# Kernel tuning notes

Hardware: AMD Instinct MI355X
Metric: run time of the kernel (lower is better)

The kernel has to match this reference:

```python
import jax, jax.numpy as jnp
import numpy as np

B, T = 1024, 128
T_IN, A_IN, V_IN = 300, 74, 35
D = 128            # dim_capsule
H = D // 2
ROUTING = 3
LABEL = 1


def _glorot(key, shape):
    fan_out, fan_in = shape[-2], shape[-1]
    s = jnp.sqrt(2.0 / (fan_in + fan_out)).astype(jnp.float32)
    return jax.random.normal(key, shape, jnp.float32) * s


def setup_inputs() -> dict:
    k = iter(jax.random.split(jax.random.key(0), 40))
    inp = {}
    inp["text"] = jax.random.normal(next(k), (B, T, T_IN), jnp.float32)
    inp["audio"] = jax.random.normal(next(k), (B, T, A_IN), jnp.float32)
    inp["video"] = jax.random.normal(next(k), (B, T, V_IN), jnp.float32)
    # bidirectional encoder LSTMs (hidden = D//2 per direction); biases b = b_ih + b_hh
    for p, din in (("t", T_IN), ("a", A_IN), ("v", V_IN)):
        for d in ("f", "b"):
            inp[p + "_Wih_" + d] = _glorot(next(k), (4 * H, din))
            inp[p + "_Whh_" + d] = _glorot(next(k), (4 * H, H))
            inp[p + "_b_" + d] = jnp.zeros((4 * H,), jnp.float32)
    # 4 capsule projection matrices per modality, stacked [4, D, D]
    inp["Wt"] = _glorot(next(k), (4, D, D))
    inp["Wa"] = _glorot(next(k), (4, D, D))
    inp["Wv"] = _glorot(next(k), (4, D, D))
    # routing LSTMs (ta, tv, av, tav) stacked on leading axis
    inp["r_Wih"] = _glorot(next(k), (4, 4 * D, D))
    inp["r_Whh"] = _glorot(next(k), (4, 4 * D, D))
    inp["r_b"] = jnp.zeros((4, 4 * D), jnp.float32)
    # decision bidirectional LSTM (hidden = D per direction)
    for d in ("f", "b"):
        inp["d_Wih_" + d] = _glorot(next(k), (4 * D, D))
        inp["d_Whh_" + d] = _glorot(next(k), (4 * D, D))
        inp["d_b_" + d] = jnp.zeros((4 * D,), jnp.float32)
    inp["fc1_W"] = _glorot(next(k), (H, D))
    inp["fc1_b"] = jnp.zeros((H,), jnp.float32)
    inp["fc2_W"] = _glorot(next(k), (LABEL, H))
    inp["fc2_b"] = jnp.zeros((LABEL,), jnp.float32)
    inp["batch_size"] = B
    return inp


def _lstm_final(x, Wih, Whh, b):
    # x: [B, T, I] -> final hidden state [B, Hh]; torch gate order i, f, g, o
    Hh = Whh.shape[-1]
    z = jnp.zeros((x.shape[0], Hh), x.dtype)

    def step(carry, xt):
        h, c = carry
        g = xt @ Wih.T + h @ Whh.T + b
        i, f, gg, o = jnp.split(g, 4, axis=-1)
        c = jax.nn.sigmoid(f) * c + jax.nn.sigmoid(i) * jnp.tanh(gg)
        h = jax.nn.sigmoid(o) * jnp.tanh(c)
        return (h, c), None

    (h, _), _ = jax.lax.scan(step, (z, z), jnp.swapaxes(x, 0, 1))
    return h


def _forward(text, audio, video,
             t_Wih_f, t_Whh_f, t_b_f, t_Wih_b, t_Whh_b, t_b_b,
             a_Wih_f, a_Whh_f, a_b_f, a_Wih_b, a_Whh_b, a_b_b,
             v_Wih_f, v_Whh_f, v_b_f, v_Wih_b, v_Whh_b, v_b_b,
             Wt, Wa, Wv, r_Wih, r_Whh, r_b,
             d_Wih_f, d_Whh_f, d_b_f, d_Wih_b, d_Whh_b, d_b_b,
             fc1_W, fc1_b, fc2_W, fc2_b):
    Bsz = text.shape[0]

    def ctx(x, Wf, Uf, bf, Wb, Ub, bb):
        # biLSTM final hidden, fwd||bwd concat -> [B, 1, D]
        hf = _lstm_final(x, Wf, Uf, bf)
        hb = _lstm_final(x[:, ::-1], Wb, Ub, bb)
        return jnp.concatenate([hf, hb], -1)[:, None, :]

    tc = ctx(text, t_Wih_f, t_Whh_f, t_b_f, t_Wih_b, t_Whh_b, t_b_b)
    ac = ctx(audio, a_Wih_f, a_Whh_f, a_b_f, a_Wih_b, a_Whh_b, a_b_b)
    vc = ctx(video, v_Wih_f, v_Whh_f, v_b_f, v_Wih_b, v_Whh_b, v_b_b)

    tusc = jnp.einsum('bod,kde->kboe', tc, Wt)   # [4, B, 1, D]
    ausc = jnp.einsum('bod,kde->kboe', ac, Wa)
    vusc = jnp.einsum('bod,kde->kboe', vc, Wv)

    pre = [jnp.concatenate([tusc[0], ausc[0]], 1),                # ta  [B,2,D]
           jnp.concatenate([tusc[1], vusc[0]], 1),                # tv  [B,2,D]
           jnp.concatenate([ausc[1], vusc[1]], 1),                # av  [B,2,D]
           jnp.concatenate([tusc[2], ausc[2], vusc[2]], 1)]       # tav [B,3,D]

    rc = [jnp.ones((Bsz, n, D), text.dtype) for n in (2, 2, 2, 3, 7)]
    dc = None
    for r in range(ROUTING + 1):
        rc = [jax.nn.softmax(c, axis=1) for c in rc]
        # per-pair routing LSTMs, final hidden [B,1,D]
        bc = [_lstm_final(rc[i] * pre[i], r_Wih[i], r_Whh[i], r_b[i])[:, None, :]
              for i in range(4)]
        deci = jnp.concatenate([tusc[3], ausc[3], vusc[3]] + bc, 1)  # [B,7,D]
        xd = rc[4] * deci
        # decision biLSTM: sum of both directions' final hidden -> [B,1,D]
        dc = (_lstm_final(xd, d_Wih_f, d_Whh_f, d_b_f)
              + _lstm_final(xd[:, ::-1], d_Wih_b, d_Whh_b, d_b_b))[:, None, :]
        if r < ROUTING:
            # agreement update: bmm gives [B,n,1], broadcasts over last dim (== repeat)
            rc = [rc[i] + jnp.matmul(pre[i], jnp.swapaxes(bc[i], 1, 2)) for i in range(4)] \
                 + [rc[4] + jnp.matmul(deci, jnp.swapaxes(dc, 1, 2))]

    dc = dc[:, 0, :]
    o1 = jnp.tanh(dc @ fc1_W.T + fc1_b)
    return o1 @ fc2_W.T + fc2_b   # mosi: no output tanh


def reference(text, audio, video,
              t_Wih_f, t_Whh_f, t_b_f, t_Wih_b, t_Whh_b, t_b_b,
              a_Wih_f, a_Whh_f, a_b_f, a_Wih_b, a_Whh_b, a_b_b,
              v_Wih_f, v_Whh_f, v_b_f, v_Wih_b, v_Whh_b, v_b_b,
              Wt, Wa, Wv, r_Wih, r_Whh, r_b,
              d_Wih_f, d_Whh_f, d_b_f, d_Wih_b, d_Whh_b, d_b_b,
              fc1_W, fc1_b, fc2_W, fc2_b, batch_size):
    return _forward(text, audio, video,
                    t_Wih_f, t_Whh_f, t_b_f, t_Wih_b, t_Whh_b, t_b_b,
                    a_Wih_f, a_Whh_f, a_b_f, a_Wih_b, a_Whh_b, a_b_b,
                    v_Wih_f, v_Whh_f, v_b_f, v_Wih_b, v_Whh_b, v_b_b,
                    Wt, Wa, Wv, r_Wih, r_Whh, r_b,
                    d_Wih_f, d_Whh_f, d_b_f, d_Wih_b, d_Whh_b, d_b_b,
                    fc1_W, fc1_b, fc2_W, fc2_b)
```

## Files before the change

### kernel.cpp

```cpp
#include <hip/hip_runtime.h>

typedef __bf16 bf16;
typedef _Float16 f16;
typedef f16 f16x8 __attribute__((ext_vector_type(8)));
typedef float f32x4 __attribute__((ext_vector_type(4)));

__device__ __forceinline__ f32x4 mfma16h(f16x8 a, f16x8 b, f32x4 c) {
  return __builtin_amdgcn_mfma_f32_16x16x32_f16(a, b, c, 0, 0, 0);
}
__device__ __forceinline__ float sigm(float x) { return 1.0f / (1.0f + __expf(-x)); }
__device__ __forceinline__ float tanh_f(float x) {
  float e = __expf(-2.0f * fabsf(x));
  return copysignf((1.0f - e) / (1.0f + e), x);
}
__device__ __forceinline__ float ldin(const void* p, long i, int f32m) {
  if (f32m) return ((const float*)p)[i];
  unsigned u = (unsigned)((const unsigned short*)p)[i] << 16;
  return __uint_as_float(u);
}
__device__ __forceinline__ unsigned short f16u(f16 h) { return __builtin_bit_cast(unsigned short, h); }
__device__ __forceinline__ float bfc(unsigned short s) { return __uint_as_float((unsigned)s << 16); }

__global__ void detect_dtype(const unsigned short* __restrict__ p, int* __restrict__ flag) {
  __shared__ int cnt;
  if (threadIdx.x == 0) cnt = 0;
  __syncthreads();
  int c = 0;
  for (int i = threadIdx.x; i < 4096; i += 256) {
    unsigned e = (p[2 * i] >> 7) & 0xFFu;
    if (e >= 0xC0u) ++c;
  }
  atomicAdd(&cnt, c);
  __syncthreads();
  if (threadIdx.x == 0) *flag = (cnt > 64) ? 1 : 0;
}


struct PadArgs { const void* src[6]; };
__global__ void conv_pad(PadArgs a, f16* __restrict__ wo, const int* __restrict__ flag) {
  const int dinT[6] = {300, 300, 74, 74, 35, 35};
  const int kpT[6] = {320, 320, 96, 96, 64, 64};
  const int offT[6] = {0, 81920, 163840, 188416, 212992, 229376};
  int id = blockIdx.y;
  int din = dinT[id], kp = kpT[id];
  const void* s = a.src[id];
  f16* o = wo + offT[id];
  int f32m = *flag;
  int total = 256 * kp;
  for (int i = blockIdx.x * blockDim.x + threadIdx.x; i < total; i += gridDim.x * blockDim.x) {
    int n = i / kp, k = i - n * kp;
    float v = (k < din) ? ldin(s, n * din + k, f32m) : 0.0f;
    o[i] = (f16)v;
  }
}

struct HiloArgs { const void* src[12]; int n[12]; int off[12]; };
__global__ void conv_h16(HiloArgs a, f16* __restrict__ wo, const int* __restrict__ flag) {
  int j = blockIdx.y;
  int n = a.n[j];
  const void* s = a.src[j];
  f16* o = wo + a.off[j];
  int f32m = *flag;
  for (int i = blockIdx.x * blockDim.x + threadIdx.x; i < n; i += gridDim.x * blockDim.x)
    o[i] = (f16)ldin(s, i, f32m);
}

struct F32Args { const void* src[16]; int n[16]; int off[16]; };
__global__ void conv_f32(F32Args a, float* __restrict__ dst, const int* __restrict__ flag) {
  int j = blockIdx.y;
  int n = a.n[j];
  const void* s = a.src[j];
  float* d = dst + a.off[j];
  int f32m = *flag;
  for (int i = blockIdx.x * blockDim.x + threadIdx.x; i < n; i += gridDim.x * blockDim.x)
    d[i] = ldin(s, i, f32m);
}

__global__ void init_rc(float* __restrict__ rcs) {
  int i = blockIdx.x * 256 + threadIdx.x;
  if (i < 16384) rcs[i] = 1.0f;
}

struct TriArgs {
  const void* x[3];
  const f16* wAll;
  const float* fmisc;
  float* ctx;
  const int* flag;
};

template <int DIN, int KP, int CHUNK, int F32M>
__device__ void tri_body(const void* __restrict__ xsrc,
                         const f16* __restrict__ wp, const f16* __restrict__ whh,
                         const float* __restrict__ bias, float* __restrict__ ctx,
                         int m, int d, int b0, char* sm) {
  constexpr int XP = KP + 8;
  constexpr int NKS = KP / 32;
  constexpr int NCH = DIN / CHUNK;
  constexpr int ITER = (NCH + 7) / 8;

  f16 (*Xhi)[XP] = (f16 (*)[XP])sm;
  f16 (*Xlo)[XP] = (f16 (*)[XP])(sm + 32 * XP * 2);
  f16 (*hbuf)[16][72] = (f16 (*)[16][72])(sm + 64 * XP * 2);

  const int tid = threadIdx.x;
  const int lane = tid & 63, n16 = lane & 15, q = lane >> 4, w = tid >> 6;
  const int u = w * 16 + n16;
  const int srow = tid & 31, sct = tid >> 5;

  {
    unsigned* z = (unsigned*)sm;
    int nz = (64 * XP * 2 + 4608) >> 2;
    for (int i = tid; i < nz; i += 256) z[i] = 0u;
  }

  f16x8 wf[4][2];
#pragma unroll
  for (int g = 0; g < 4; ++g)
#pragma unroll
    for (int ks = 0; ks < 2; ++ks)
      wf[g][ks] = *(const f16x8*)(whh + (g * 64 + u) * 64 + ks * 32 + q * 8);
  float bg[4];
#pragma unroll
  for (int g = 0; g < 4; ++g) bg[g] = bias[g * 64 + u];

  uint4 pf[ITER];
  auto stage_load = [&](int tg) {
#pragma unroll
    for (int i = 0; i < ITER; ++i) {
      int c = sct + i * 8;
      if (c < NCH) {
        int tl = srow >> 4, bb = srow & 15;
        int t = tg * 2 + tl; if (d) t = 127 - t;
        long base = ((long)(b0 + bb) * 128 + t) * DIN + c * CHUNK;
        if (F32M) {
          const float* p = (const float*)xsrc + base;
          if constexpr (CHUNK == 4) pf[i] = *(const uint4*)p;
          else if constexpr (CHUNK == 2) { uint2 v = *(const uint2*)p; pf[i].x = v.x; pf[i].y = v.y; }
          else pf[i].x = *(const unsigned*)p;
        } else {
          const unsigned short* p = (const unsigned short*)xsrc + base;
          if constexpr (CHUNK == 4) { uint2 v = *(const uint2*)p; pf[i].x = v.x; pf[i].y = v.y; }
          else if constexpr (CHUNK == 2) pf[i].x = *(const unsigned*)p;
          else pf[i].x = *p;
        }
      }
    }
  };
  auto stage_store = [&]() {
#pragma unroll
    for (int i = 0; i < ITER; ++i) {
      int c = sct + i * 8;
      if (c < NCH) {
        float v[4];
        if (F32M) {
          v[0] = __uint_as_float(pf[i].x); v[1] = __uint_as_float(pf[i].y);
          v[2] = __uint_as_float(pf[i].z); v[3] = __uint_as_float(pf[i].w);
        } else {
          v[0] = bfc((unsigned short)(pf[i].x & 0xFFFF));
          v[1] = bfc((unsigned short)(pf[i].x >> 16));
          v[2] = bfc((unsigned short)(pf[i].y & 0xFFFF));
          v[3] = bfc((unsigned short)(pf[i].y >> 16));
        }
        unsigned short hb[4], lb[4];
#pragma unroll
        for (int e = 0; e < CHUNK; ++e) {
          f16 h = (f16)v[e];
          hb[e] = f16u(h);
          lb[e] = f16u((f16)(v[e] - (float)h));
        }
        if constexpr (CHUNK == 4) {
          uint2 H; H.x = hb[0] | ((unsigned)hb[1] << 16); H.y = hb[2] | ((unsigned)hb[3] << 16);
          *(uint2*)&Xhi[srow][c * 4] = H;
          if (F32M) {
            uint2 L; L.x = lb[0] | ((unsigned)lb[1] << 16); L.y = lb[2] | ((unsigned)lb[3] << 16);
            *(uint2*)&Xlo[srow][c * 4] = L;
          }
        } else if constexpr (CHUNK == 2) {
          *(unsigned*)&Xhi[srow][c * 2] = hb[0] | ((unsigned)hb[1] << 16);
          if (F32M) *(unsigned*)&Xlo[srow][c * 2] = lb[0] | ((unsigned)lb[1] << 16);
        } else {
          *(unsigned short*)&Xhi[srow][c] = hb[0];
          if (F32M) *(unsigned short*)&Xlo[srow][c] = lb[0];
        }
      }
    }
  };

  float c4[4] = {0.f, 0.f, 0.f, 0.f};
  int par = 0;
  stage_load(0);
  __syncthreads();

  for (int tg = 0; tg < 64; ++tg) {
    stage_store();
    if (tg < 63) stage_load(tg + 1);
    __syncthreads();

    f32x4 acc[2][4];
    const f32x4 zf = {0.f, 0.f, 0.f, 0.f};
#pragma unroll
    for (int rt = 0; rt < 2; ++rt)
#pragma unroll
      for (int g = 0; g < 4; ++g) acc[rt][g] = zf;

#pragma unroll
    for (int ks = 0; ks < NKS; ++ks) {
      f16x8 ah0 = *(const f16x8*)(&Xhi[n16][ks * 32 + q * 8]);
      f16x8 ah1 = *(const f16x8*)(&Xhi[16 + n16][ks * 32 + q * 8]);
      f16x8 al0, al1;
      if (F32M) {
        al0 = *(const f16x8*)(&Xlo[n16][ks * 32 + q * 8]);
        al1 = *(const f16x8*)(&Xlo[16 + n16][ks * 32 + q * 8]);
      }
#pragma unroll
      for (int g = 0; g < 4; ++g) {
        f16x8 bh = *(const f16x8*)(wp + (g * 64 + u) * KP + ks * 32 + q * 8);
        acc[0][g] = mfma16h(ah0, bh, acc[0][g]);
        acc[1][g] = mfma16h(ah1, bh, acc[1][g]);
        if (F32M) {
          acc[0][g] = mfma16h(al0, bh, acc[0][g]);
          acc[1][g] = mfma16h(al1, bh, acc[1][g]);
        }
      }
    }

#pragma unroll
    for (int tl = 0; tl < 2; ++tl) {
#pragma unroll
      for (int ks = 0; ks < 2; ++ks) {
        f16x8 ah = *(const f16x8*)(&hbuf[par][n16][ks * 32 + q * 8]);
#pragma unroll
        for (int g = 0; g < 4; ++g) acc[tl][g] = mfma16h(ah, wf[g][ks], acc[tl][g]);
      }
      const bool lastStep = (tg == 63) && (tl == 1);
#pragma unroll
      for (int e = 0; e < 4; ++e) {
        int row = q * 4 + e;
        float gi = acc[tl][0][e] + bg[0];
        float gf = acc[tl][1][e] + bg[1];
        float gg = acc[tl][2][e] + bg[2];
        float go = acc[tl][3][e] + bg[3];
        float c = sigm(gf) * c4[e] + sigm(gi) * tanh_f(gg);
        c4[e] = c;
        float h = sigm(go) * tanh_f(c);
        hbuf[par ^ 1][row][u] = (f16)h;
        if (lastStep) ctx[(m * 1024 + b0 + row) * 128 + d * 64 + u] = h;
      }
      par ^= 1;
      __syncthreads();
    }
  }
}

__global__ __launch_bounds__(256) void tri_lstm(TriArgs A) {
  __shared__ __align__(16) char sm[64 * 328 * 2 + 4608];
  int bid = blockIdx.x;
  int md = bid >> 6, xb = bid & 63;
  int m = md >> 1, d = md & 1, b0 = xb * 16;
  const int wpOffT[6] = {0, 81920, 163840, 188416, 212992, 229376};
  const f16* wp = A.wAll + wpOffT[md];
  const f16* whh = A.wAll + 245760 + md * 16384;
  const float* bias = A.fmisc + md * 256;
  int f32m = *A.flag;
  if (f32m) {
    if (m == 0)      tri_body<300, 320, 4, 1>(A.x[0], wp, whh, bias, A.ctx, m, d, b0, sm);
    else if (m == 1) tri_body<74, 96, 2, 1>(A.x[1], wp, whh, bias, A.ctx, m, d, b0, sm);
    else             tri_body<35, 64, 1, 1>(A.x[2], wp, whh, bias, A.ctx, m, d, b0, sm);
  } else {
    if (m == 0)      tri_body<300, 320, 4, 0>(A.x[0], wp, whh, bias, A.ctx, m, d, b0, sm);
    else if (m == 1) tri_body<74, 96, 2, 0>(A.x[1], wp, whh, bias, A.ctx, m, d, b0, sm);
    else             tri_body<35, 64, 1, 0>(A.x[2], wp, whh, bias, A.ctx, m, d, b0, sm);
  }
}

__global__ __launch_bounds__(128) void usc_kern(const float* __restrict__ ctx,
                                                const float* __restrict__ fmisc,
                                                float* __restrict__ usc) {
  __shared__ float cr[4][128];
  int b0 = blockIdx.x * 4;
  int mk = blockIdx.y, mod = mk >> 2;
  int e = threadIdx.x;
  const float* W = fmisc + 4608 + mk * 16384;
  for (int i = e; i < 512; i += 128) {
    int r = i >> 7, dd = i & 127;
    cr[r][dd] = ctx[(mod * 1024 + b0 + r) * 128 + dd];
  }
  __syncthreads();
  float a0 = 0.f, a1 = 0.f, a2 = 0.f, a3 = 0.f;
  for (int dd = 0; dd < 128; ++dd) {
    float wv = W[dd * 128 + e];
    a0 += cr[0][dd] * wv; a1 += cr[1][dd] * wv;
    a2 += cr[2][dd] * wv; a3 += cr[3][dd] * wv;
  }
  usc[(mk * 1024 + b0 + 0) * 128 + e] = a0;
  usc[(mk * 1024 + b0 + 1) * 128 + e] = a1;
  usc[(mk * 1024 + b0 + 2) * 128 + e] = a2;
  usc[(mk * 1024 + b0 + 3) * 128 + e] = a3;
}

#define LSTM_STEP_DECL \
  const int tid = threadIdx.x; \
  const int lane = tid & 63, n16 = lane & 15, q = lane >> 4, w = tid >> 6; \
  const int u = w * 16 + n16; \
  const int u2 = tid & 127, rgg = tid >> 7;

__device__ __forceinline__ void lstm_step_mfma(
    f32x4* acc, const f16 (*xh)[16][136], const f16 (*xl)[16][136],
    const f16 (*hh)[16][136], int p,
    const f16* __restrict__ Wih, const f16x8 (*whf)[4],
    int n16, int q, int u) {
#pragma unroll
  for (int ks = 0; ks < 4; ++ks) {
    f16x8 axh = *(const f16x8*)(&xh[p][n16][ks * 32 + q * 8]);
    f16x8 axl = *(const f16x8*)(&xl[p][n16][ks * 32 + q * 8]);
    f16x8 ahh = *(const f16x8*)(&hh[p][n16][ks * 32 + q * 8]);
#pragma unroll
    for (int g = 0; g < 4; ++g) {
      f16x8 bh = *(const f16x8*)(Wih + (g * 128 + u) * 128 + ks * 32 + q * 8);
      acc[g] = mfma16h(axh, bh, acc[g]);
      acc[g] = mfma16h(axl, bh, acc[g]);
      acc[g] = mfma16h(ahh, whf[g][ks], acc[g]);
    }
  }
}

__global__ __launch_bounds__(512) void rchain(const float* __restrict__ usc,
                                              const float* __restrict__ rcs,
                                              const f16* __restrict__ wAll,
                                              const float* __restrict__ fmisc,
                                              float* __restrict__ bcg) {
  __shared__ __align__(16) f16 xh[2][16][136], xl[2][16][136], hh[2][16][136];
  __shared__ float rcl[16][3];
  LSTM_STEP_DECL
  const int chain = blockIdx.y;
  const int b0 = blockIdx.x * 16;
  const int WihOff[4] = {344064, 409600, 475136, 540672};
  const int WhhOff[4] = {606208, 671744, 737280, 802816};
  const int bOff[4] = {1536, 2048, 2560, 3072};
  const int ns = (chain == 3) ? 3 : 2;

  if (tid < 16) {
    int row = tid;
    int goff = (chain == 3) ? 6 : chain * 2;
    float v[3], mx = -1e30f;
    for (int j = 0; j < ns; ++j) { v[j] = rcs[(b0 + row) * 16 + goff + j]; mx = fmaxf(mx, v[j]); }
    float s = 0.f;
    for (int j = 0; j < ns; ++j) { v[j] = __expf(v[j] - mx); s += v[j]; }
    float inv = 1.0f / s;
    for (int j = 0; j < ns; ++j) rcl[row][j] = v[j] * inv;
  }
  for (int i = tid; i < 2 * 16 * 136; i += 512) (&hh[0][0][0])[i] = (f16)0.0f;

  const f16* Whh = wAll + WhhOff[chain];
  f16x8 whf[4][4];
#pragma unroll
  for (int g = 0; g < 4; ++g)
#pragma unroll
    for (int ks = 0; ks < 4; ++ks)
      whf[g][ks] = *(const f16x8*)(Whh + (g * 128 + u) * 128 + ks * 32 + q * 8);
  const f16* Wih = wAll + WihOff[chain];
  const float* bias = fmisc + bOff[chain];
  float bg[4];
#pragma unroll
  for (int g = 0; g < 4; ++g) bg[g] = bias[g * 128 + u];

  const int preMk0[4] = {0, 1, 5, 2};
  const int preMk1[4] = {4, 8, 9, 6};
  float creg[4] = {0.f, 0.f, 0.f, 0.f};
  __syncthreads();

  for (int s = 0; s < ns; ++s) {
    int p = s & 1;
    int mk = (s == 0) ? preMk0[chain] : (s == 1 ? preMk1[chain] : 10);
#pragma unroll
    for (int rr = 0; rr < 4; ++rr) {
      int row = rgg * 4 + rr;
      float pv = usc[(mk * 1024 + b0 + row) * 128 + u2];
      float xv = rcl[row][s] * pv;
      f16 xhv = (f16)xv;
      xh[p][row][u2] = xhv;
      xl[p][row][u2] = (f16)(xv - (float)xhv);
    }
    __syncthreads();
    f32x4 acc[4];
    const f32x4 zf = {0.f, 0.f, 0.f, 0.f};
#pragma unroll
    for (int g = 0; g < 4; ++g) acc[g] = zf;
    lstm_step_mfma(acc, xh, xl, hh, p, Wih, whf, n16, q, u);
#pragma unroll
    for (int e = 0; e < 4; ++e) {
      int row = q * 4 + e;
      float gi = acc[0][e] + bg[0];
      float gf = acc[1][e] + bg[1];
      float gg = acc[2][e] + bg[2];
      float go = acc[3][e] + bg[3];
      float c = sigm(gf) * creg[e] + sigm(gi) * tanh_f(gg);
      creg[e] = c;
      float h = sigm(go) * tanh_f(c);
      hh[p ^ 1][row][u] = (f16)h;
      if (s == ns - 1) bcg[(chain * 1024 + b0 + row) * 128 + u] = h;
    }
  }
}

__global__ __launch_bounds__(512) void decision(const float* __restrict__ usc,
                                                const float* __restrict__ rcs,
                                                const f16* __restrict__ wAll,
                                                const float* __restrict__ fmisc,
                                                const float* __restrict__ bcg,
                                                float* __restrict__ dcF,
                                                float* __restrict__ dcB) {
  __shared__ __align__(16) f16 xh[2][16][136], xl[2][16][136], hh[2][16][136];
  __shared__ float rcl[16][7];
  LSTM_STEP_DECL
  const int dir = blockIdx.y;
  const int b0 = blockIdx.x * 16;

  if (tid < 16) {
    int row = tid;
    float v[7], mx = -1e30f;
    for (int j = 0; j < 7; ++j) { v[j] = rcs[(b0 + row) * 16 + 9 + j]; mx = fmaxf(mx, v[j]); }
    float s = 0.f;
    for (int j = 0; j < 7; ++j) { v[j] = __expf(v[j] - mx); s += v[j]; }
    float inv = 1.0f / s;
    for (int j = 0; j < 7; ++j) rcl[row][j] = v[j] * inv;
  }
  for (int i = tid; i < 2 * 16 * 136; i += 512) (&hh[0][0][0])[i] = (f16)0.0f;

  const int WihOffD[2] = {868352, 999424};
  const int WhhOffD[2] = {933888, 1064960};
  const int bOffD[2] = {3584, 4096};
  const f16* Whh = wAll + WhhOffD[dir];
  f16x8 whf[4][4];
#pragma unroll
  for (int g = 0; g < 4; ++g)
#pragma unroll
    for (int ks = 0; ks < 4; ++ks)
      whf[g][ks] = *(const f16x8*)(Whh + (g * 128 + u) * 128 + ks * 32 + q * 8);
  const f16* Wih = wAll + WihOffD[dir];
  const float* bias = fmisc + bOffD[dir];
  float bg[4];
#pragma unroll
  for (int g = 0; g < 4; ++g) bg[g] = bias[g * 128 + u];

  const int dmk[3] = {3, 7, 11};
  float creg[4] = {0.f, 0.f, 0.f, 0.f};
  __syncthreads();

  for (int s = 0; s < 7; ++s) {
    int p = s & 1;
    int j = dir ? (6 - s) : s;
#pragma unroll
    for (int rr = 0; rr < 4; ++rr) {
      int row = rgg * 4 + rr;
      float pv = (j < 3) ? usc[(dmk[j] * 1024 + b0 + row) * 128 + u2]
                         : bcg[((j - 3) * 1024 + b0 + row) * 128 + u2];
      float xv = rcl[row][j] * pv;
      f16 xhv = (f16)xv;
      xh[p][row][u2] = xhv;
      xl[p][row][u2] = (f16)(xv - (float)xhv);
    }
    __syncthreads();
    f32x4 acc[4];
    const f32x4 zf = {0.f, 0.f, 0.f, 0.f};
#pragma unroll
    for (int g = 0; g < 4; ++g) acc[g] = zf;
    lstm_step_mfma(acc, xh, xl, hh, p, Wih, whf, n16, q, u);
#pragma unroll
    for (int e = 0; e < 4; ++e) {
      int row = q * 4 + e;
      float gi = acc[0][e] + bg[0];
      float gf = acc[1][e] + bg[1];
      float gg = acc[2][e] + bg[2];
      float go = acc[3][e] + bg[3];
      float c = sigm(gf) * creg[e] + sigm(gi) * tanh_f(gg);
      creg[e] = c;
      float h = sigm(go) * tanh_f(c);
      hh[p ^ 1][row][u] = (f16)h;
      if (s == 6) {
        if (dir == 0) dcF[(b0 + row) * 128 + u] = h;
        else dcB[(b0 + row) * 128 + u] = h;
      }
    }
  }
}

__global__ __launch_bounds__(256) void rupdate(const float* __restrict__ usc,
                                               const float* __restrict__ bcg,
                                               const float* __restrict__ dcF,
                                               const float* __restrict__ dcB,
                                               float* __restrict__ rcs,
                                               float* __restrict__ dcw, int last) {
  __shared__ float dsum[16][128];
  __shared__ float rcl[16][16];
  const int tid = threadIdx.x;
  const int b0 = blockIdx.x * 16;
  for (int i = tid; i < 2048; i += 256) {
    int row = i >> 7, col = i & 127;
    float v = dcF[(b0 + row) * 128 + col] + dcB[(b0 + row) * 128 + col];
    dsum[row][col] = v;
    if (last) dcw[(b0 + row) * 128 + col] = v;
  }
  {
    int row = tid >> 4, cap = tid & 15;
    rcl[row][cap] = rcs[(b0 + row) * 16 + cap];
  }
  __syncthreads();
  if (!last) {
    int row = tid >> 4, cap = tid & 15;
    const int goffT[16] = {0, 0, 2, 2, 4, 4, 6, 6, 6, 9, 9, 9, 9, 9, 9, 9};
    const int gnT[16] = {2, 2, 2, 2, 2, 2, 3, 3, 3, 7, 7, 7, 7, 7, 7, 7};
    int go = goffT[cap], gn = gnT[cap];
    float mx = -1e30f;
    for (int j = 0; j < gn; ++j) mx = fmaxf(mx, rcl[row][go + j]);
    float s = 0.f;
    for (int j = 0; j < gn; ++j) s += __expf(rcl[row][go + j] - mx);
    float sm = __expf(rcl[row][cap] - mx) / s;

    const int preMkTab[9] = {0, 4, 1, 8, 5, 9, 2, 6, 10};
    float a = 0.f;
    if (cap < 9) {
      int i = (cap < 6) ? (cap >> 1) : 3;
      const float* pr = usc + (preMkTab[cap] * 1024 + b0 + row) * 128;
      const float* bcrow = bcg + (i * 1024 + b0 + row) * 128;
      for (int dd = 0; dd < 128; ++dd) a += pr[dd] * bcrow[dd];
    } else {
      int j = cap - 9;
      if (j < 3) {
        const int dmk[3] = {3, 7, 11};
        const float* pr = usc + (dmk[j] * 1024 + b0 + row) * 128;
        for (int dd = 0; dd < 128; ++dd) a += pr[dd] * dsum[row][dd];
      } else {
        const float* bcrow = bcg + ((j - 3) * 1024 + b0 + row) * 128;
        for (int dd = 0; dd < 128; ++dd) a += bcrow[dd] * dsum[row][dd];
      }
    }
    rcs[(b0 + row) * 16 + cap] = sm + a;
  }
}

__global__ __launch_bounds__(64) void head(const float* __restrict__ dc, const float* __restrict__ fcw,
                                           void* __restrict__ out, const int* __restrict__ flag) {
  int b = blockIdx.x, j = threadIdx.x;
  const float* r = dc + b * 128;
  float acc = fcw[209408 + j];
  for (int dd = 0; dd < 128; ++dd) acc += r[dd] * fcw[201216 + j * 128 + dd];
  float o = tanh_f(acc) * fcw[209472 + j];
  for (int off = 32; off; off >>= 1) o += __shfl_down(o, off, 64);
  if (j == 0) {
    float res = o + fcw[209536];
    if (*flag) ((float*)out)[b] = res;
    else ((bf16*)out)[b] = (bf16)res;
  }
}

extern "C" void kernel_launch(void* const* d_in, const int* in_sizes, int n_in,
                              void* d_out, int out_size, void* d_ws, size_t ws_size,
                              hipStream_t stream) {
  float* fw = (float*)d_ws;
  int* flag = (int*)d_ws;
  float* ctx = fw + 4;
  float* usc = ctx + 393216;
  float* dcw = usc + 1572864;
  float* fmisc = dcw + 131072;
  float* rcs = fmisc + 209552;
  float* bcg = rcs + 16384;
  float* dcF = bcg + 524288;
  float* dcB = dcF + 131072;
  f16* wAll = (f16*)(dcB + 131072);

  hipLaunchKernelGGL(detect_dtype, dim3(1), dim3(256), 0, stream,
                     (const unsigned short*)d_in[0], flag);

  PadArgs pa;
  HiloArgs ha;
  for (int m = 0; m < 3; ++m)
    for (int dd = 0; dd < 2; ++dd) {
      int md = m * 6 + dd * 3;
      pa.src[m * 2 + dd] = d_in[3 + md + 0];
      ha.src[m * 2 + dd] = d_in[3 + md + 1];
      ha.n[m * 2 + dd] = 16384;
      ha.off[m * 2 + dd] = 245760 + (m * 2 + dd) * 16384;
    }
  const int hsrc[6] = {24, 25, 27, 28, 30, 31};
  const int hn[6] = {262144, 262144, 65536, 65536, 65536, 65536};
  const int hoff[6] = {344064, 606208, 868352, 933888, 999424, 1064960};
  for (int j = 0; j < 6; ++j) { ha.src[6 + j] = d_in[hsrc[j]]; ha.n[6 + j] = hn[j]; ha.off[6 + j] = hoff[j]; }
  hipLaunchKernelGGL(conv_pad, dim3(64, 6), dim3(256), 0, stream, pa, wAll, (const int*)flag);
  hipLaunchKernelGGL(conv_h16, dim3(128, 12), dim3(256), 0, stream, ha, wAll, (const int*)flag);

  F32Args fa;
  for (int m = 0; m < 3; ++m)
    for (int dd = 0; dd < 2; ++dd) {
      fa.src[m * 2 + dd] = d_in[3 + m * 6 + dd * 3 + 2];
      fa.n[m * 2 + dd] = 256;
      fa.off[m * 2 + dd] = (m * 2 + dd) * 256;
    }
  const int fsrc[10] = {26, 29, 32, 21, 22, 23, 33, 34, 35, 36};
  const int fn[10] = {2048, 512, 512, 65536, 65536, 65536, 8192, 64, 64, 1};
  const int foff[10] = {1536, 3584, 4096, 4608, 70144, 135680, 201216, 209408, 209472, 209536};
  for (int j = 0; j < 10; ++j) { fa.src[6 + j] = d_in[fsrc[j]]; fa.n[6 + j] = fn[j]; fa.off[6 + j] = foff[j]; }
  hipLaunchKernelGGL(conv_f32, dim3(64, 16), dim3(256), 0, stream, fa, fmisc, (const int*)flag);
  hipLaunchKernelGGL(init_rc, dim3(64), dim3(256), 0, stream, rcs);

  TriArgs ta;
  ta.x[0] = d_in[0]; ta.x[1] = d_in[1]; ta.x[2] = d_in[2];
  ta.wAll = wAll; ta.fmisc = fmisc; ta.ctx = ctx; ta.flag = flag;
  hipLaunchKernelGGL(tri_lstm, dim3(384), dim3(256), 0, stream, ta);

  hipLaunchKernelGGL(usc_kern, dim3(256, 12), dim3(128), 0, stream,
                     (const float*)ctx, (const float*)fmisc, usc);

  for (int r = 0; r < 4; ++r) {
    hipLaunchKernelGGL(rchain, dim3(64, 4), dim3(512), 0, stream,
                       (const float*)usc, (const float*)rcs, (const f16*)wAll,
                       (const float*)fmisc, bcg);
    hipLaunchKernelGGL(decision, dim3(64, 2), dim3(512), 0, stream,
                       (const float*)usc, (const float*)rcs, (const f16*)wAll,
                       (const float*)fmisc, (const float*)bcg, dcF, dcB);
    hipLaunchKernelGGL(rupdate, dim3(64), dim3(256), 0, stream,
                       (const float*)usc, (const float*)bcg, (const float*)dcF,
                       (const float*)dcB, rcs, dcw, (r == 3) ? 1 : 0);
  }

  hipLaunchKernelGGL(head, dim3(1024), dim3(64), 0, stream,
                     (const float*)dcw, (const float*)fmisc, d_out, (const int*)flag);
}
```

Measured before the change: 910.2 us.

## Split encoder LSTM input projection across two warp groups per block

```diff
diff --git a/kernel.cpp b/kernel.cpp
--- a/kernel.cpp
+++ b/kernel.cpp
@@ -97,21 +97,23 @@
   constexpr int XP = KP + 8;
   constexpr int NKS = KP / 32;
   constexpr int NCH = DIN / CHUNK;
-  constexpr int ITER = (NCH + 7) / 8;
+  constexpr int ITER = (NCH + 15) / 16;
 
   f16 (*Xhi)[XP] = (f16 (*)[XP])sm;
   f16 (*Xlo)[XP] = (f16 (*)[XP])(sm + 32 * XP * 2);
   f16 (*hbuf)[16][72] = (f16 (*)[16][72])(sm + 64 * XP * 2);
+  float (*accb)[64][16] = (float (*)[64][16])(sm + 64 * XP * 2 + 4608);
 
   const int tid = threadIdx.x;
-  const int lane = tid & 63, n16 = lane & 15, q = lane >> 4, w = tid >> 6;
+  const int grp = tid >> 8;
+  const int lane = tid & 63, n16 = lane & 15, q = lane >> 4, w = (tid >> 6) & 3;
   const int u = w * 16 + n16;
   const int srow = tid & 31, sct = tid >> 5;
 
   {
     unsigned* z = (unsigned*)sm;
     int nz = (64 * XP * 2 + 4608) >> 2;
-    for (int i = tid; i < nz; i += 256) z[i] = 0u;
+    for (int i = tid; i < nz; i += 512) z[i] = 0u;
   }
 
   f16x8 wf[4][2];
@@ -128,7 +130,7 @@
   auto stage_load = [&](int tg) {
 #pragma unroll
     for (int i = 0; i < ITER; ++i) {
-      int c = sct + i * 8;
+      int c = sct + i * 16;
       if (c < NCH) {
         int tl = srow >> 4, bb = srow & 15;
         int t = tg * 2 + tl; if (d) t = 127 - t;
@@ -150,7 +152,7 @@
   auto stage_store = [&]() {
 #pragma unroll
     for (int i = 0; i < ITER; ++i) {
-      int c = sct + i * 8;
+      int c = sct + i * 16;
       if (c < NCH) {
         float v[4];
         if (F32M) {
@@ -192,60 +194,67 @@
   stage_load(0);
   __syncthreads();
 
+  const int xr = grp * 16 + n16;
+
   for (int tg = 0; tg < 64; ++tg) {
     stage_store();
     if (tg < 63) stage_load(tg + 1);
     __syncthreads();
 
-    f32x4 acc[2][4];
+    f32x4 acc[4];
     const f32x4 zf = {0.f, 0.f, 0.f, 0.f};
 #pragma unroll
-    for (int rt = 0; rt < 2; ++rt)
-#pragma unroll
-      for (int g = 0; g < 4; ++g) acc[rt][g] = zf;
+    for (int g = 0; g < 4; ++g) acc[g] = zf;
 
 #pragma unroll
     for (int ks = 0; ks < NKS; ++ks) {
-      f16x8 ah0 = *(const f16x8*)(&Xhi[n16][ks * 32 + q * 8]);
-      f16x8 ah1 = *(const f16x8*)(&Xhi[16 + n16][ks * 32 + q * 8]);
-      f16x8 al0, al1;
-      if (F32M) {
-        al0 = *(const f16x8*)(&Xlo[n16][ks * 32 + q * 8]);
-        al1 = *(const f16x8*)(&Xlo[16 + n16][ks * 32 + q * 8]);
-      }
+      f16x8 ah = *(const f16x8*)(&Xhi[xr][ks * 32 + q * 8]);
+      f16x8 al;
+      if (F32M) al = *(const f16x8*)(&Xlo[xr][ks * 32 + q * 8]);
 #pragma unroll
       for (int g = 0; g < 4; ++g) {
         f16x8 bh = *(const f16x8*)(wp + (g * 64 + u) * KP + ks * 32 + q * 8);
-        acc[0][g] = mfma16h(ah0, bh, acc[0][g]);
-        acc[1][g] = mfma16h(ah1, bh, acc[1][g]);
-        if (F32M) {
-          acc[0][g] = mfma16h(al0, bh, acc[0][g]);
-          acc[1][g] = mfma16h(al1, bh, acc[1][g]);
+        acc[g] = mfma16h(ah, bh, acc[g]);
+        if (F32M) acc[g] = mfma16h(al, bh, acc[g]);
+      }
+    }
+    if (grp == 1) {
+#pragma unroll
+      for (int g = 0; g < 4; ++g)
+        *(f32x4*)(&accb[g][u][q * 4]) = acc[g];
+    }
+
+#pragma unroll
+    for (int tl = 0; tl < 2; ++tl) {
+      if (grp == 0) {
+        f32x4 a2[4];
+        if (tl == 0) {
+#pragma unroll
+          for (int g = 0; g < 4; ++g) a2[g] = acc[g];
+        } else {
+#pragma unroll
+          for (int g = 0; g < 4; ++g) a2[g] = *(const f32x4*)(&accb[g][u][q * 4]);
         }
-      }
-    }
-
-#pragma unroll
-    for (int tl = 0; tl < 2; ++tl) {
-#pragma unroll
-      for (int ks = 0; ks < 2; ++ks) {
-        f16x8 ah = *(const f16x8*)(&hbuf[par][n16][ks * 32 + q * 8]);
-#pragma unroll
-        for (int g = 0; g < 4; ++g) acc[tl][g] = mfma16h(ah, wf[g][ks], acc[tl][g]);
-      }
-      const bool lastStep = (tg == 63) && (tl == 1);
-#pragma unroll
-      for (int e = 0; e < 4; ++e) {
-        int row = q * 4 + e;
-        float gi = acc[tl][0][e] + bg[0];
-        float gf = acc[tl][1][e] + bg[1];
-        float gg = acc[tl][2][e] + bg[2];
-        float go = acc[tl][3][e] + bg[3];
-        float c = sigm(gf) * c4[e] + sigm(gi) * tanh_f(gg);
-        c4[e] = c;
-        float h = sigm(go) * tanh_f(c);
-        hbuf[par ^ 1][row][u] = (f16)h;
-        if (lastStep) ctx[(m * 1024 + b0 + row) * 128 + d * 64 + u] = h;
+#pragma unroll
+        for (int ks = 0; ks < 2; ++ks) {
+          f16x8 ah = *(const f16x8*)(&hbuf[par][n16][ks * 32 + q * 8]);
+#pragma unroll
+          for (int g = 0; g < 4; ++g) a2[g] = mfma16h(ah, wf[g][ks], a2[g]);
+        }
+        const bool lastStep = (tg == 63) && (tl == 1);
+#pragma unroll
+        for (int e = 0; e < 4; ++e) {
+          int row = q * 4 + e;
+          float gi = a2[0][e] + bg[0];
+          float gf = a2[1][e] + bg[1];
+          float gg = a2[2][e] + bg[2];
+          float go = a2[3][e] + bg[3];
+          float c = sigm(gf) * c4[e] + sigm(gi) * tanh_f(gg);
+          c4[e] = c;
+          float h = sigm(go) * tanh_f(c);
+          hbuf[par ^ 1][row][u] = (f16)h;
+          if (lastStep) ctx[(m * 1024 + b0 + row) * 128 + d * 64 + u] = h;
+        }
       }
       par ^= 1;
       __syncthreads();
@@ -253,8 +262,8 @@
   }
 }
 
-__global__ __launch_bounds__(256) void tri_lstm(TriArgs A) {
-  __shared__ __align__(16) char sm[64 * 328 * 2 + 4608];
+__global__ __launch_bounds__(512) void tri_lstm(TriArgs A) {
+  __shared__ __align__(16) char sm[64 * 328 * 2 + 4608 + 16384];
   int bid = blockIdx.x;
   int md = bid >> 6, xb = bid & 63;
   int m = md >> 1, d = md & 1, b0 = xb * 16;
@@ -607,7 +616,7 @@
   TriArgs ta;
   ta.x[0] = d_in[0]; ta.x[1] = d_in[1]; ta.x[2] = d_in[2];
   ta.wAll = wAll; ta.fmisc = fmisc; ta.ctx = ctx; ta.flag = flag;
-  hipLaunchKernelGGL(tri_lstm, dim3(384), dim3(256), 0, stream, ta);
+  hipLaunchKernelGGL(tri_lstm, dim3(384), dim3(512), 0, stream, ta);
 
   hipLaunchKernelGGL(usc_kern, dim3(256, 12), dim3(128), 0, stream,
                      (const float*)ctx, (const float*)fmisc, usc);
```

Measured after the change: 872.2 us. -4.2%, faster.

## Double tri_lstm block to 512 threads with register-resident input weights and shared gate exchange

Applied to the files above, without the earlier changes.

```diff
diff --git a/kernel.cpp b/kernel.cpp
--- a/kernel.cpp
+++ b/kernel.cpp
@@ -97,38 +97,45 @@
   constexpr int XP = KP + 8;
   constexpr int NKS = KP / 32;
   constexpr int NCH = DIN / CHUNK;
-  constexpr int ITER = (NCH + 7) / 8;
+  constexpr int ITER = (NCH + 15) / 16;
 
   f16 (*Xhi)[XP] = (f16 (*)[XP])sm;
   f16 (*Xlo)[XP] = (f16 (*)[XP])(sm + 32 * XP * 2);
   f16 (*hbuf)[16][72] = (f16 (*)[16][72])(sm + 64 * XP * 2);
+  float* gbuf = (float*)(sm + 64 * XP * 2 + 4608);
 
   const int tid = threadIdx.x;
-  const int lane = tid & 63, n16 = lane & 15, q = lane >> 4, w = tid >> 6;
-  const int u = w * 16 + n16;
+  const int lane = tid & 63, n16 = lane & 15, q = lane >> 4, w8 = tid >> 6;
   const int srow = tid & 31, sct = tid >> 5;
+  const int hc = tid & 63, rr = tid >> 6;
+
+  f16x8 wihr[2][NKS];
+  f16x8 whr[2][2];
+#pragma unroll
+  for (int t = 0; t < 2; ++t) {
+    int cc = (w8 + t * 8) * 16 + n16;
+#pragma unroll
+    for (int ks = 0; ks < NKS; ++ks)
+      wihr[t][ks] = *(const f16x8*)(wp + cc * KP + ks * 32 + q * 8);
+#pragma unroll
+    for (int ks = 0; ks < 2; ++ks)
+      whr[t][ks] = *(const f16x8*)(whh + cc * 64 + ks * 32 + q * 8);
+  }
+  float bgm[4];
+#pragma unroll
+  for (int g = 0; g < 4; ++g) bgm[g] = bias[g * 64 + hc];
 
   {
     unsigned* z = (unsigned*)sm;
     int nz = (64 * XP * 2 + 4608) >> 2;
-    for (int i = tid; i < nz; i += 256) z[i] = 0u;
-  }
-
-  f16x8 wf[4][2];
-#pragma unroll
-  for (int g = 0; g < 4; ++g)
-#pragma unroll
-    for (int ks = 0; ks < 2; ++ks)
-      wf[g][ks] = *(const f16x8*)(whh + (g * 64 + u) * 64 + ks * 32 + q * 8);
-  float bg[4];
-#pragma unroll
-  for (int g = 0; g < 4; ++g) bg[g] = bias[g * 64 + u];
+    for (int i = tid; i < nz; i += 512) z[i] = 0u;
+  }
 
   uint4 pf[ITER];
   auto stage_load = [&](int tg) {
 #pragma unroll
     for (int i = 0; i < ITER; ++i) {
-      int c = sct + i * 8;
+      int c = sct + i * 16;
       if (c < NCH) {
         int tl = srow >> 4, bb = srow & 15;
         int t = tg * 2 + tl; if (d) t = 127 - t;
@@ -150,7 +157,7 @@
   auto stage_store = [&]() {
 #pragma unroll
     for (int i = 0; i < ITER; ++i) {
-      int c = sct + i * 8;
+      int c = sct + i * 16;
       if (c < NCH) {
         float v[4];
         if (F32M) {
@@ -187,8 +194,7 @@
     }
   };
 
-  float c4[4] = {0.f, 0.f, 0.f, 0.f};
-  int par = 0;
+  float c2[2] = {0.f, 0.f};
   stage_load(0);
   __syncthreads();
 
@@ -197,64 +203,88 @@
     if (tg < 63) stage_load(tg + 1);
     __syncthreads();
 
-    f32x4 acc[2][4];
-    const f32x4 zf = {0.f, 0.f, 0.f, 0.f};
-#pragma unroll
-    for (int rt = 0; rt < 2; ++rt)
-#pragma unroll
-      for (int g = 0; g < 4; ++g) acc[rt][g] = zf;
-
+    f32x4 a00, a01, a10, a11;
+    {
+      const f32x4 zf = {0.f, 0.f, 0.f, 0.f};
+      a00 = zf; a01 = zf; a10 = zf; a11 = zf;
+    }
 #pragma unroll
     for (int ks = 0; ks < NKS; ++ks) {
       f16x8 ah0 = *(const f16x8*)(&Xhi[n16][ks * 32 + q * 8]);
       f16x8 ah1 = *(const f16x8*)(&Xhi[16 + n16][ks * 32 + q * 8]);
-      f16x8 al0, al1;
+      a00 = mfma16h(ah0, wihr[0][ks], a00);
+      a01 = mfma16h(ah0, wihr[1][ks], a01);
+      a10 = mfma16h(ah1, wihr[0][ks], a10);
+      a11 = mfma16h(ah1, wihr[1][ks], a11);
       if (F32M) {
-        al0 = *(const f16x8*)(&Xlo[n16][ks * 32 + q * 8]);
-        al1 = *(const f16x8*)(&Xlo[16 + n16][ks * 32 + q * 8]);
+        f16x8 al0 = *(const f16x8*)(&Xlo[n16][ks * 32 + q * 8]);
+        f16x8 al1 = *(const f16x8*)(&Xlo[16 + n16][ks * 32 + q * 8]);
+        a00 = mfma16h(al0, wihr[0][ks], a00);
+        a01 = mfma16h(al0, wihr[1][ks], a01);
+        a10 = mfma16h(al1, wihr[0][ks], a10);
+        a11 = mfma16h(al1, wihr[1][ks], a11);
       }
-#pragma unroll
-      for (int g = 0; g < 4; ++g) {
-        f16x8 bh = *(const f16x8*)(wp + (g * 64 + u) * KP + ks * 32 + q * 8);
-        acc[0][g] = mfma16h(ah0, bh, acc[0][g]);
-        acc[1][g] = mfma16h(ah1, bh, acc[1][g]);
-        if (F32M) {
-          acc[0][g] = mfma16h(al0, bh, acc[0][g]);
-          acc[1][g] = mfma16h(al1, bh, acc[1][g]);
-        }
-      }
-    }
-
-#pragma unroll
-    for (int tl = 0; tl < 2; ++tl) {
-#pragma unroll
-      for (int ks = 0; ks < 2; ++ks) {
-        f16x8 ah = *(const f16x8*)(&hbuf[par][n16][ks * 32 + q * 8]);
-#pragma unroll
-        for (int g = 0; g < 4; ++g) acc[tl][g] = mfma16h(ah, wf[g][ks], acc[tl][g]);
-      }
-      const bool lastStep = (tg == 63) && (tl == 1);
-#pragma unroll
-      for (int e = 0; e < 4; ++e) {
-        int row = q * 4 + e;
-        float gi = acc[tl][0][e] + bg[0];
-        float gf = acc[tl][1][e] + bg[1];
-        float gg = acc[tl][2][e] + bg[2];
-        float go = acc[tl][3][e] + bg[3];
-        float c = sigm(gf) * c4[e] + sigm(gi) * tanh_f(gg);
-        c4[e] = c;
-        float h = sigm(go) * tanh_f(c);
-        hbuf[par ^ 1][row][u] = (f16)h;
-        if (lastStep) ctx[(m * 1024 + b0 + row) * 128 + d * 64 + u] = h;
-      }
-      par ^= 1;
-      __syncthreads();
-    }
-  }
-}
-
-__global__ __launch_bounds__(256) void tri_lstm(TriArgs A) {
-  __shared__ __align__(16) char sm[64 * 328 * 2 + 4608];
+    }
+
+    {
+      f16x8 h0 = *(const f16x8*)(&hbuf[0][n16][q * 8]);
+      f16x8 h1 = *(const f16x8*)(&hbuf[0][n16][32 + q * 8]);
+      a00 = mfma16h(h0, whr[0][0], a00); a00 = mfma16h(h1, whr[0][1], a00);
+      a01 = mfma16h(h0, whr[1][0], a01); a01 = mfma16h(h1, whr[1][1], a01);
+    }
+#pragma unroll
+    for (int e = 0; e < 4; ++e) {
+      gbuf[(q * 4 + e) * 260 + w8 * 16 + n16] = a00[e];
+      gbuf[(q * 4 + e) * 260 + 128 + w8 * 16 + n16] = a01[e];
+    }
+    __syncthreads();
+
+#pragma unroll
+    for (int e = 0; e < 2; ++e) {
+      int row = rr + e * 8;
+      float gi = gbuf[row * 260 + hc] + bgm[0];
+      float gf = gbuf[row * 260 + 64 + hc] + bgm[1];
+      float gg = gbuf[row * 260 + 128 + hc] + bgm[2];
+      float go = gbuf[row * 260 + 192 + hc] + bgm[3];
+      float c = sigm(gf) * c2[e] + sigm(gi) * tanh_f(gg);
+      c2[e] = c;
+      float h = sigm(go) * tanh_f(c);
+      hbuf[1][row][hc] = (f16)h;
+    }
+    __syncthreads();
+
+    {
+      f16x8 h0 = *(const f16x8*)(&hbuf[1][n16][q * 8]);
+      f16x8 h1 = *(const f16x8*)(&hbuf[1][n16][32 + q * 8]);
+      a10 = mfma16h(h0, whr[0][0], a10); a10 = mfma16h(h1, whr[0][1], a10);
+      a11 = mfma16h(h0, whr[1][0], a11); a11 = mfma16h(h1, whr[1][1], a11);
+    }
+#pragma unroll
+    for (int e = 0; e < 4; ++e) {
+      gbuf[(q * 4 + e) * 260 + w8 * 16 + n16] = a10[e];
+      gbuf[(q * 4 + e) * 260 + 128 + w8 * 16 + n16] = a11[e];
+    }
+    __syncthreads();
+
+    const bool lastStep = (tg == 63);
+#pragma unroll
+    for (int e = 0; e < 2; ++e) {
+      int row = rr + e * 8;
+      float gi = gbuf[row * 260 + hc] + bgm[0];
+      float gf = gbuf[row * 260 + 64 + hc] + bgm[1];
+      float gg = gbuf[row * 260 + 128 + hc] + bgm[2];
+      float go = gbuf[row * 260 + 192 + hc] + bgm[3];
+      float c = sigm(gf) * c2[e] + sigm(gi) * tanh_f(gg);
+      c2[e] = c;
+      float h = sigm(go) * tanh_f(c);
+      hbuf[0][row][hc] = (f16)h;
+      if (lastStep) ctx[(m * 1024 + b0 + row) * 128 + d * 64 + hc] = h;
+    }
+  }
+}
+
+__global__ __launch_bounds__(512, 2) void tri_lstm(TriArgs A) {
+  __shared__ __align__(16) char sm[64 * 328 * 2 + 4608 + 16640];
   int bid = blockIdx.x;
   int md = bid >> 6, xb = bid & 63;
   int m = md >> 1, d = md & 1, b0 = xb * 16;
@@ -607,7 +637,7 @@
   TriArgs ta;
   ta.x[0] = d_in[0]; ta.x[1] = d_in[1]; ta.x[2] = d_in[2];
   ta.wAll = wAll; ta.fmisc = fmisc; ta.ctx = ctx; ta.flag = flag;
-  hipLaunchKernelGGL(tri_lstm, dim3(384), dim3(256), 0, stream, ta);
+  hipLaunchKernelGGL(tri_lstm, dim3(384), dim3(512), 0, stream, ta);
 
   hipLaunchKernelGGL(usc_kern, dim3(256, 12), dim3(128), 0, stream,
                      (const float*)ctx, (const float*)fmisc, usc);
```

After: 848.2 us. 6.8% less time.
